# Kernel optimization log

Hardware: AMD Instinct MI355X
Metric: run time of the kernel (lower is better)

Reference implementation:

```python
import jax, jax.numpy as jnp
import numpy as np

EMBED_DIM = 128
TEMP_DIM = EMBED_DIM // 4  # 32
NUM_TYPES = 50
DATE_SCALE = 1825.0
LN_EPS = 1e-5


def _layernorm(x, w, b):
    m = jnp.mean(x, axis=-1, keepdims=True)
    v = jnp.mean((x - m) ** 2, axis=-1, keepdims=True)
    return (x - m) * jax.lax.rsqrt(v + LN_EPS) * w + b


def setup_inputs() -> dict:
    key = jax.random.key(0)
    ks = jax.random.split(key, 16)
    B, L = 4096, 200
    inp = {
        "treatment_ids": jax.random.randint(ks[0], (B, L), 0, NUM_TYPES, dtype=jnp.int64 if jax.config.jax_enable_x64 else jnp.int32),
        "dates": jax.random.uniform(ks[1], (B, L), dtype=jnp.float32) * DATE_SCALE,
        "lengths": jax.random.randint(ks[2], (B,), 0, L + 1, dtype=jnp.int32),
        # parameters
        "emb": jax.random.normal(ks[3], (NUM_TYPES, EMBED_DIM), jnp.float32),
        "tp_w": jax.random.normal(ks[4], (1, TEMP_DIM), jnp.float32) * 0.1,
        "tp_b": jnp.zeros((TEMP_DIM,), jnp.float32),
        "tp_lnw": jnp.ones((TEMP_DIM,), jnp.float32),
        "tp_lnb": jnp.zeros((TEMP_DIM,), jnp.float32),
        "w1": jax.random.normal(ks[5], (EMBED_DIM + TEMP_DIM, EMBED_DIM), jnp.float32) * 0.05,
        "b1": jnp.zeros((EMBED_DIM,), jnp.float32),
        "ln1w": jnp.ones((EMBED_DIM,), jnp.float32),
        "ln1b": jnp.zeros((EMBED_DIM,), jnp.float32),
        "w2": jax.random.normal(ks[6], (EMBED_DIM, EMBED_DIM), jnp.float32) * 0.05,
        "b2": jnp.zeros((EMBED_DIM,), jnp.float32),
        "ln2w": jnp.ones((EMBED_DIM,), jnp.float32),
        "ln2b": jnp.zeros((EMBED_DIM,), jnp.float32),
    }
    return inp


def reference(treatment_ids, dates, lengths, emb, tp_w, tp_b, tp_lnw, tp_lnb,
              w1, b1, ln1w, ln1b, w2, b2, ln2w, ln2b):
    B, L = treatment_ids.shape
    mask = (jnp.arange(L)[None, :] < lengths[:, None]).astype(dates.dtype)  # [B, L]

    # embedding lookup [B, L, D]
    treat = emb[treatment_ids]

    # temporal projection: Linear(1 -> D/4) + LN + GELU
    dn = (dates / DATE_SCALE)[..., None]                      # [B, L, 1]
    temporal = dn * tp_w[0] + tp_b                            # [B, L, D/4]
    temporal = jax.nn.gelu(_layernorm(temporal, tp_lnw, tp_lnb), approximate=False)

    combined = jnp.concatenate([treat, temporal], axis=-1)    # [B, L, D + D/4]

    # sequence encoder (dropout is identity at eval)
    h = jnp.einsum("blk,kd->bld", combined, w1) + b1
    h = jax.nn.gelu(_layernorm(h, ln1w, ln1b), approximate=False)
    h = jnp.einsum("blk,kd->bld", h, w2) + b2
    h = _layernorm(h, ln2w, ln2b)                             # [B, L, D]

    # masked mean pool; empty histories -> zeros
    counts = jnp.sum(mask, axis=1, keepdims=True)             # [B, 1]
    pooled = jnp.sum(h * mask[..., None], axis=1) / jnp.maximum(counts, 1.0)
    return jnp.where(counts > 0, pooled, 0.0)                 # [B, D]
```

## Files before the change

kernel.cpp:

```cpp
#include <hip/hip_runtime.h>
#include <cmath>

#define LN_EPS 1e-5f

typedef float  f32x4  __attribute__((ext_vector_type(4)));
typedef short  short8 __attribute__((ext_vector_type(8)));
typedef unsigned int uint4v __attribute__((ext_vector_type(4)));

#define W1TF_U4 512
#define W2F_U4  2048
#define E1_U4   1650
#define WLDS_U4 2560

__device__ __forceinline__ unsigned short f32_bf16_rne(float f) {
    union { float f; unsigned u; } v; v.f = f;
    unsigned r = v.u + 0x7FFFu + ((v.u >> 16) & 1u);
    return (unsigned short)(r >> 16);
}

__device__ __forceinline__ unsigned cvt_pk_bf16(float lo, float hi) {
    unsigned r;
    asm("v_cvt_pk_bf16_f32 %0, %1, %2" : "=v"(r) : "v"(lo), "v"(hi));
    return r;
}

__device__ __forceinline__ float gelu_f(float x) {
    float ax = fabsf(x);
    float a  = ax * 0.70710678118654752f;
    float t  = __builtin_amdgcn_rcpf(fmaf(0.3275911f, a, 1.0f));
    float p  = t * fmaf(t, fmaf(t, fmaf(t, fmaf(t, 1.061405429f, -1.453152027f),
                                        1.421413741f), -0.284496736f), 0.254829592f);
    float e  = __builtin_amdgcn_exp2f(-1.44269504089f * a * a);
    float E  = fmaf(-p, e, 1.0f);
    return 0.5f * fmaf(ax, E, x);
}

template<int C>
__device__ __forceinline__ float dpp_radd(float x) {
    int t = __builtin_amdgcn_update_dpp(0, __builtin_bit_cast(int, x), C, 0xF, 0xF, true);
    return x + __builtin_bit_cast(float, t);
}
__device__ __forceinline__ float red16(float x) {
    x = dpp_radd<0x128>(x);
    x = dpp_radd<0x124>(x);
    x = dpp_radd<0x122>(x);
    x = dpp_radd<0x121>(x);
    return x;
}

__global__ void prep_kernel(const float* __restrict__ w1, const float* __restrict__ w2,
                            const float* __restrict__ emb,
                            const float* __restrict__ tp_w, const float* __restrict__ tp_b,
                            unsigned* __restrict__ ws) {
    const int tid = blockIdx.x * 256 + threadIdx.x;
    uint4v* w1tf = (uint4v*)ws;
    uint4v* w2f  = w1tf + W1TF_U4;
    float*  E1   = (float*)(w2f + W2F_U4);
    float*  tps  = E1 + 6600;

    for (int i = tid; i < W1TF_U4; i += 8192) {
        const int lane = i & 63, nt = i >> 6;
        const int k0 = 128 + (lane >> 4) * 8, n = nt * 16 + (lane & 15);
        uint4v r;
        #pragma unroll
        for (int j2 = 0; j2 < 4; ++j2) {
            unsigned lo = f32_bf16_rne(w1[(k0 + 2 * j2) * 128 + n]);
            unsigned hi = f32_bf16_rne(w1[(k0 + 2 * j2 + 1) * 128 + n]);
            r[j2] = lo | (hi << 16);
        }
        w1tf[i] = r;
    }
    for (int i = tid; i < W2F_U4; i += 8192) {
        const int lane = i & 63, nt = (i >> 6) & 7, kt = i >> 9;
        const int k0 = kt * 32 + (lane >> 4) * 8, n = nt * 16 + (lane & 15);
        uint4v r;
        #pragma unroll
        for (int j2 = 0; j2 < 4; ++j2) {
            unsigned lo = f32_bf16_rne(w2[(k0 + 2 * j2) * 128 + n]);
            unsigned hi = f32_bf16_rne(w2[(k0 + 2 * j2 + 1) * 128 + n]);
            r[j2] = lo | (hi << 16);
        }
        w2f[i] = r;
    }
    if (tid < 6400) {
        const int t = tid >> 7, n = tid & 127;
        float s = 0.f;
        #pragma unroll 4
        for (int k = 0; k < 128; ++k)
            s = fmaf(emb[t * 128 + k], w1[k * 128 + n], s);
        E1[t * 132 + n] = s;
    }
    if (tid == 0) {
        float Sw = 0.f, Sb = 0.f, Sww = 0.f, Swb = 0.f, Sbb = 0.f;
        for (int j = 0; j < 32; ++j) {
            const float ww = tp_w[j], bb = tp_b[j];
            Sw += ww; Sb += bb; Sww += ww * ww; Swb += ww * bb; Sbb += bb * bb;
        }
        tps[0] = Sw; tps[1] = Sb; tps[2] = Sww; tps[3] = Swb; tps[4] = Sbb;
    }
}

__global__ __launch_bounds__(1024, 4) void encoder_mfma(
    const int*   __restrict__ tids,  const float* __restrict__ dates,
    const int*   __restrict__ lengths,
    const float* __restrict__ tp_w,  const float* __restrict__ tp_b,
    const float* __restrict__ tp_lnw,const float* __restrict__ tp_lnb,
    const float* __restrict__ b1,    const float* __restrict__ ln1w, const float* __restrict__ ln1b,
    const float* __restrict__ b2,    const float* __restrict__ ln2w, const float* __restrict__ ln2b,
    const unsigned* __restrict__ ws, float* __restrict__ out,
    int B, int L)
{
    __shared__ __align__(16) uint4v wlds[WLDS_U4];
    __shared__ __align__(16) float  E1lds[6600];
    __shared__ __align__(16) unsigned short a2[16][4][64][8];
    __shared__ float poolrow[4][128];
    __shared__ __align__(16) f32x4 tcoef[32];
    __shared__ __align__(16) f32x4 ecoef1[128];
    __shared__ __align__(16) f32x4 ecoef2[128];

    const int tid = threadIdx.x;
    const int lane = tid & 63, w = tid >> 6;
    const int c = lane & 15, g = lane >> 4;
    const int b0 = blockIdx.x * 4;

    for (int i = tid; i < WLDS_U4; i += 1024)
        wlds[i] = ((const uint4v*)ws)[i];
    for (int i = tid; i < E1_U4; i += 1024)
        ((uint4v*)E1lds)[i] = ((const uint4v*)ws)[WLDS_U4 + i];
    if (tid < 512) poolrow[tid >> 7][tid & 127] = 0.f;

    const float* tps = (const float*)((const uint4v*)ws + WLDS_U4 + E1_U4);

    if (tid < 32)  tcoef[tid]  = (f32x4){tp_w[tid], tp_b[tid], tp_lnw[tid], tp_lnb[tid]};
    if (tid < 128) {
        ecoef1[tid] = (f32x4){b1[tid], ln1w[tid], ln1b[tid], 0.f};
        ecoef2[tid] = (f32x4){b2[tid], ln2w[tid], ln2b[tid], 0.f};
    }
    __syncthreads();

    const float Sw = tps[0], Sb = tps[1], Sww = tps[2], Swb = tps[3], Sbb = tps[4];

    const int len0 = (b0 + 0 < B) ? min(max(lengths[b0 + 0], 0), L) : 0;
    const int len1 = (b0 + 1 < B) ? min(max(lengths[b0 + 1], 0), L) : 0;
    const int len2 = (b0 + 2 < B) ? min(max(lengths[b0 + 2], 0), L) : 0;
    const int len3 = (b0 + 3 < B) ? min(max(lengths[b0 + 3], 0), L) : 0;
    const int nt0 = (len0 + 15) >> 4, nt1 = (len1 + 15) >> 4;
    const int nt2 = (len2 + 15) >> 4, nt3 = (len3 + 15) >> 4;
    const int cum1 = nt0, cum2 = nt0 + nt1, cum3 = cum2 + nt2, T = cum3 + nt3;

    const int srl = lane ^ ((lane >> 3) & 3);

    for (int t = w; t < T; t += 16) {
        int row, tl, lenr;
        if (t >= cum3)      { row = 3; tl = t - cum3; lenr = len3; }
        else if (t >= cum2) { row = 2; tl = t - cum2; lenr = len2; }
        else if (t >= cum1) { row = 1; tl = t - cum1; lenr = len1; }
        else                { row = 0; tl = t;        lenr = len0; }
        const int R0 = tl << 4;
        const long base = (long)(b0 + row) * L;

        const int pc = min(R0 + c, L - 1);
        const float d = dates[base + pc] * (1.f / 1825.f);
        int idr[4];
        #pragma unroll
        for (int r = 0; r < 4; ++r)
            idr[r] = tids[base + min(R0 + 4 * g + r, L - 1)];

        short8 tfrag;
        {
            const float tm = fmaf(d, Sw, Sb) * (1.f / 32.f);
            float tv = fmaf(d * d, Sww, fmaf(2.f * d, Swb, Sbb)) * (1.f / 32.f) - tm * tm;
            const float trs = rsqrtf(fmaxf(tv, 0.f) + LN_EPS);
            const int j0 = g * 8;
            uint4v r;
            #pragma unroll
            for (int j2 = 0; j2 < 4; ++j2) {
                const f32x4 t0 = tcoef[j0 + 2*j2];
                const f32x4 t1 = tcoef[j0 + 2*j2 + 1];
                const float y0 = fmaf((fmaf(d, t0[0], t0[1]) - tm) * trs, t0[2], t0[3]);
                const float y1 = fmaf((fmaf(d, t1[0], t1[1]) - tm) * trs, t1[2], t1[3]);
                r[j2] = cvt_pk_bf16(gelu_f(y0), gelu_f(y1));
            }
            union { uint4v u; short8 s; } cv; cv.u = r;
            tfrag = cv.s;
        }

        f32x4 acc[8];
        #pragma unroll
        for (int r = 0; r < 4; ++r) {
            const int e1base = idr[r] * 132 + c;
            #pragma unroll
            for (int nt = 0; nt < 8; ++nt)
                acc[nt][r] = E1lds[e1base + nt * 16];
        }
        __builtin_amdgcn_s_setprio(1);
        #pragma unroll
        for (int nt = 0; nt < 8; ++nt) {
            const short8 bf = ((const short8*)wlds)[nt * 64 + lane];
            acc[nt] = __builtin_amdgcn_mfma_f32_16x16x32_bf16(tfrag, bf, acc[nt], 0, 0, 0);
        }
        __builtin_amdgcn_s_setprio(0);

        {
            f32x4 e1[8];
            #pragma unroll
            for (int nt = 0; nt < 8; ++nt) e1[nt] = ecoef1[nt * 16 + c];
            #pragma unroll
            for (int r = 0; r < 4; ++r) {
                float v[8], s = 0.f, q = 0.f;
                #pragma unroll
                for (int nt = 0; nt < 8; ++nt) {
                    v[nt] = acc[nt][r] + e1[nt][0];
                    s += v[nt]; q = fmaf(v[nt], v[nt], q);
                }
                s = red16(s); q = red16(q);
                const float mean = s * (1.f / 128.f);
                const float var  = fmaxf(q * (1.f / 128.f) - mean * mean, 0.f);
                const float rstd = rsqrtf(var + LN_EPS);
                const int mrow = 4 * g + r;
                #pragma unroll
                for (int n2 = 0; n2 < 4; ++n2) {
                    const float y0 = gelu_f(fmaf((v[2*n2]   - mean) * rstd, e1[2*n2][1],   e1[2*n2][2]));
                    const float y1 = gelu_f(fmaf((v[2*n2+1] - mean) * rstd, e1[2*n2+1][1], e1[2*n2+1][2]));
                    const unsigned pk = cvt_pk_bf16(y0, y1);
                    {
                        const int kcol  = (2*n2) * 16 + c;
                        const int row64 = ((kcol >> 3) & 3) * 16 + mrow;
                        const int srow  = row64 ^ ((row64 >> 3) & 3);
                        a2[w][kcol >> 5][srow][kcol & 7] = (unsigned short)(pk & 0xffffu);
                    }
                    {
                        const int kcol  = (2*n2+1) * 16 + c;
                        const int row64 = ((kcol >> 3) & 3) * 16 + mrow;
                        const int srow  = row64 ^ ((row64 >> 3) & 3);
                        a2[w][kcol >> 5][srow][kcol & 7] = (unsigned short)(pk >> 16);
                    }
                }
            }
        }

        asm volatile("" ::: "memory");

        f32x4 acc2[8];
        #pragma unroll
        for (int nt = 0; nt < 8; ++nt) acc2[nt] = (f32x4){0.f, 0.f, 0.f, 0.f};
        __builtin_amdgcn_s_setprio(1);
        #pragma unroll
        for (int kt2 = 0; kt2 < 4; ++kt2) {
            short8 af;
            __builtin_memcpy(&af, &a2[w][kt2][srl][0], 16);
            #pragma unroll
            for (int nt = 0; nt < 8; ++nt) {
                const short8 bf = ((const short8*)(wlds + W1TF_U4))[(kt2 * 8 + nt) * 64 + lane];
                acc2[nt] = __builtin_amdgcn_mfma_f32_16x16x32_bf16(af, bf, acc2[nt], 0, 0, 0);
            }
        }
        __builtin_amdgcn_s_setprio(0);

        asm volatile("" ::: "memory");

        {
            f32x4 e2[8];
            #pragma unroll
            for (int nt = 0; nt < 8; ++nt) e2[nt] = ecoef2[nt * 16 + c];
            float ptile[8];
            #pragma unroll
            for (int nt = 0; nt < 8; ++nt) ptile[nt] = 0.f;
            #pragma unroll
            for (int r = 0; r < 4; ++r) {
                float v[8], s = 0.f, q = 0.f;
                #pragma unroll
                for (int nt = 0; nt < 8; ++nt) {
                    v[nt] = acc2[nt][r] + e2[nt][0];
                    s += v[nt]; q = fmaf(v[nt], v[nt], q);
                }
                s = red16(s); q = red16(q);
                const float mean = s * (1.f / 128.f);
                const float var  = fmaxf(q * (1.f / 128.f) - mean * mean, 0.f);
                const float rstd = rsqrtf(var + LN_EPS);
                const float msk = ((R0 + 4 * g + r) < lenr) ? 1.f : 0.f;
                #pragma unroll
                for (int nt = 0; nt < 8; ++nt) {
                    const float y = fmaf((v[nt] - mean) * rstd, e2[nt][1], e2[nt][2]);
                    ptile[nt] = fmaf(y, msk, ptile[nt]);
                }
            }
            #pragma unroll
            for (int nt = 0; nt < 8; ++nt) {
                float tv = ptile[nt];
                tv += __shfl_xor(tv, 16);
                tv += __shfl_xor(tv, 32);
                ptile[nt] = tv;
            }
            if (g == 0) {
                #pragma unroll
                for (int nt = 0; nt < 8; ++nt)
                    atomicAdd(&poolrow[row][nt * 16 + c], ptile[nt]);
            }
        }
    }

    __syncthreads();
    if (tid < 512) {
        const int r4  = tid >> 7;
        const int col = tid & 127;
        const int bo  = b0 + r4;
        if (bo < B) {
            const int lenb = min(max(lengths[bo], 0), L);
            out[bo * 128 + col] = (lenb > 0) ? poolrow[r4][col] / (float)lenb : 0.f;
        }
    }
}

extern "C" void kernel_launch(void* const* d_in, const int* in_sizes, int n_in,
                              void* d_out, int out_size, void* d_ws, size_t ws_size,
                              hipStream_t stream) {
    const int*   tids    = (const int*)  d_in[0];
    const float* dates   = (const float*)d_in[1];
    const int*   lengths = (const int*)  d_in[2];
    const float* emb     = (const float*)d_in[3];
    const float* tp_w    = (const float*)d_in[4];
    const float* tp_b    = (const float*)d_in[5];
    const float* tp_lnw  = (const float*)d_in[6];
    const float* tp_lnb  = (const float*)d_in[7];
    const float* w1      = (const float*)d_in[8];
    const float* b1      = (const float*)d_in[9];
    const float* ln1w    = (const float*)d_in[10];
    const float* ln1b    = (const float*)d_in[11];
    const float* w2      = (const float*)d_in[12];
    const float* b2      = (const float*)d_in[13];
    const float* ln2w    = (const float*)d_in[14];
    const float* ln2b    = (const float*)d_in[15];
    float* out = (float*)d_out;

    const int B = in_sizes[2];
    const int L = in_sizes[0] / B;

    hipLaunchKernelGGL(prep_kernel, dim3(32), dim3(256), 0, stream,
                       w1, w2, emb, tp_w, tp_b, (unsigned*)d_ws);
    hipLaunchKernelGGL(encoder_mfma, dim3((B + 3) / 4), dim3(1024), 0, stream,
                       tids, dates, lengths, tp_w, tp_b, tp_lnw, tp_lnb,
                       b1, ln1w, ln1b, b2, ln2w, ln2b,
                       (const unsigned*)d_ws, out, B, L);
}
```

Measured before the change: 217.0 us.

## Process 32-row tiles per wave, read E1 from global, use 768-thread blocks

Each wave now handles two 16-row M-tiles per iteration, so every B-fragment load from LDS feeds two MFMAs. The E1 table (embedding times W1) moves out of LDS and is gathered from global/L2 with stride 128. Blocks shrink to 768 threads covering 6 batch rows, with the a2 staging buffer doubled per wave. This is meant to cut LDS pressure and raise weight reuse, at the cost of more registers per wave, padding waste on the 32-row tiles, and uncached global gathers for E1.

```diff
diff --git a/kernel.cpp b/kernel.cpp
--- a/kernel.cpp
+++ b/kernel.cpp
@@ -9,7 +9,7 @@
 
 #define W1TF_U4 512
 #define W2F_U4  2048
-#define E1_U4   1650
+#define E1_U4   1600
 #define WLDS_U4 2560
 
 __device__ __forceinline__ unsigned short f32_bf16_rne(float f) {
@@ -56,7 +56,7 @@
     uint4v* w1tf = (uint4v*)ws;
     uint4v* w2f  = w1tf + W1TF_U4;
     float*  E1   = (float*)(w2f + W2F_U4);
-    float*  tps  = E1 + 6600;
+    float*  tps  = E1 + 6400;
 
     for (int i = tid; i < W1TF_U4; i += 8192) {
         const int lane = i & 63, nt = i >> 6;
@@ -88,7 +88,7 @@
         #pragma unroll 4
         for (int k = 0; k < 128; ++k)
             s = fmaf(emb[t * 128 + k], w1[k * 128 + n], s);
-        E1[t * 132 + n] = s;
+        E1[t * 128 + n] = s;
     }
     if (tid == 0) {
         float Sw = 0.f, Sb = 0.f, Sww = 0.f, Swb = 0.f, Sbb = 0.f;
@@ -100,7 +100,7 @@
     }
 }
 
-__global__ __launch_bounds__(1024, 4) void encoder_mfma(
+__global__ __launch_bounds__(768, 3) void encoder_mfma(
     const int*   __restrict__ tids,  const float* __restrict__ dates,
     const int*   __restrict__ lengths,
     const float* __restrict__ tp_w,  const float* __restrict__ tp_b,
@@ -111,9 +111,8 @@
     int B, int L)
 {
     __shared__ __align__(16) uint4v wlds[WLDS_U4];
-    __shared__ __align__(16) float  E1lds[6600];
-    __shared__ __align__(16) unsigned short a2[16][4][64][8];
-    __shared__ float poolrow[4][128];
+    __shared__ __align__(16) unsigned short a2[12][2][4][64][8];
+    __shared__ float poolrow[6][128];
     __shared__ __align__(16) f32x4 tcoef[32];
     __shared__ __align__(16) f32x4 ecoef1[128];
     __shared__ __align__(16) f32x4 ecoef2[128];
@@ -121,15 +120,14 @@
     const int tid = threadIdx.x;
     const int lane = tid & 63, w = tid >> 6;
     const int c = lane & 15, g = lane >> 4;
-    const int b0 = blockIdx.x * 4;
-
-    for (int i = tid; i < WLDS_U4; i += 1024)
+    const int b0 = blockIdx.x * 6;
+
+    for (int i = tid; i < WLDS_U4; i += 768)
         wlds[i] = ((const uint4v*)ws)[i];
-    for (int i = tid; i < E1_U4; i += 1024)
-        ((uint4v*)E1lds)[i] = ((const uint4v*)ws)[WLDS_U4 + i];
-    if (tid < 512) poolrow[tid >> 7][tid & 127] = 0.f;
-
-    const float* tps = (const float*)((const uint4v*)ws + WLDS_U4 + E1_U4);
+    poolrow[tid >> 7][tid & 127] = 0.f;
+
+    const float* E1g = (const float*)((const uint4v*)ws + WLDS_U4);
+    const float* tps = E1g + 6400;
 
     if (tid < 32)  tcoef[tid]  = (f32x4){tp_w[tid], tp_b[tid], tp_lnw[tid], tp_lnb[tid]};
     if (tid < 128) {
@@ -140,64 +138,93 @@
 
     const float Sw = tps[0], Sb = tps[1], Sww = tps[2], Swb = tps[3], Sbb = tps[4];
 
-    const int len0 = (b0 + 0 < B) ? min(max(lengths[b0 + 0], 0), L) : 0;
-    const int len1 = (b0 + 1 < B) ? min(max(lengths[b0 + 1], 0), L) : 0;
-    const int len2 = (b0 + 2 < B) ? min(max(lengths[b0 + 2], 0), L) : 0;
-    const int len3 = (b0 + 3 < B) ? min(max(lengths[b0 + 3], 0), L) : 0;
-    const int nt0 = (len0 + 15) >> 4, nt1 = (len1 + 15) >> 4;
-    const int nt2 = (len2 + 15) >> 4, nt3 = (len3 + 15) >> 4;
-    const int cum1 = nt0, cum2 = nt0 + nt1, cum3 = cum2 + nt2, T = cum3 + nt3;
+    int lenA[6];
+    #pragma unroll
+    for (int i = 0; i < 6; ++i)
+        lenA[i] = (b0 + i < B) ? min(max(lengths[b0 + i], 0), L) : 0;
+    const int n0 = (lenA[0] + 31) >> 5, n1 = (lenA[1] + 31) >> 5, n2 = (lenA[2] + 31) >> 5;
+    const int n3 = (lenA[3] + 31) >> 5, n4 = (lenA[4] + 31) >> 5, n5 = (lenA[5] + 31) >> 5;
+    const int cum1 = n0, cum2 = cum1 + n1, cum3 = cum2 + n2;
+    const int cum4 = cum3 + n3, cum5 = cum4 + n4, T = cum5 + n5;
+    const int len0 = lenA[0], len1 = lenA[1], len2 = lenA[2];
+    const int len3 = lenA[3], len4 = lenA[4], len5 = lenA[5];
 
     const int srl = lane ^ ((lane >> 3) & 3);
 
-    for (int t = w; t < T; t += 16) {
+    for (int st = w; st < T; st += 12) {
         int row, tl, lenr;
-        if (t >= cum3)      { row = 3; tl = t - cum3; lenr = len3; }
-        else if (t >= cum2) { row = 2; tl = t - cum2; lenr = len2; }
-        else if (t >= cum1) { row = 1; tl = t - cum1; lenr = len1; }
-        else                { row = 0; tl = t;        lenr = len0; }
-        const int R0 = tl << 4;
+        if      (st >= cum5) { row = 5; tl = st - cum5; lenr = len5; }
+        else if (st >= cum4) { row = 4; tl = st - cum4; lenr = len4; }
+        else if (st >= cum3) { row = 3; tl = st - cum3; lenr = len3; }
+        else if (st >= cum2) { row = 2; tl = st - cum2; lenr = len2; }
+        else if (st >= cum1) { row = 1; tl = st - cum1; lenr = len1; }
+        else                 { row = 0; tl = st;        lenr = len0; }
+        const int R0 = tl << 5;
+        const bool amt1 = (R0 + 16) < lenr;
         const long base = (long)(b0 + row) * L;
 
-        const int pc = min(R0 + c, L - 1);
-        const float d = dates[base + pc] * (1.f / 1825.f);
-        int idr[4];
+        int idr0[4], idr1[4];
         #pragma unroll
         for (int r = 0; r < 4; ++r)
-            idr[r] = tids[base + min(R0 + 4 * g + r, L - 1)];
-
-        short8 tfrag;
+            idr0[r] = tids[base + min(R0 + 4 * g + r, L - 1)];
+        if (amt1) {
+            #pragma unroll
+            for (int r = 0; r < 4; ++r)
+                idr1[r] = tids[base + min(R0 + 16 + 4 * g + r, L - 1)];
+        }
+        const float dn0 = dates[base + min(R0 + c,      L - 1)] * (1.f / 1825.f);
+        const float dn1 = dates[base + min(R0 + 16 + c, L - 1)] * (1.f / 1825.f);
+
+        f32x4 acc[2][8];
+        #pragma unroll
+        for (int r = 0; r < 4; ++r) {
+            const int e1b = idr0[r] * 128 + c;
+            #pragma unroll
+            for (int nt = 0; nt < 8; ++nt)
+                acc[0][nt][r] = E1g[e1b + nt * 16];
+        }
+        if (amt1) {
+            #pragma unroll
+            for (int r = 0; r < 4; ++r) {
+                const int e1b = idr1[r] * 128 + c;
+                #pragma unroll
+                for (int nt = 0; nt < 8; ++nt)
+                    acc[1][nt][r] = E1g[e1b + nt * 16];
+            }
+        }
+
+        short8 tfrag[2];
         {
-            const float tm = fmaf(d, Sw, Sb) * (1.f / 32.f);
-            float tv = fmaf(d * d, Sww, fmaf(2.f * d, Swb, Sbb)) * (1.f / 32.f) - tm * tm;
-            const float trs = rsqrtf(fmaxf(tv, 0.f) + LN_EPS);
             const int j0 = g * 8;
-            uint4v r;
-            #pragma unroll
-            for (int j2 = 0; j2 < 4; ++j2) {
-                const f32x4 t0 = tcoef[j0 + 2*j2];
-                const f32x4 t1 = tcoef[j0 + 2*j2 + 1];
-                const float y0 = fmaf((fmaf(d, t0[0], t0[1]) - tm) * trs, t0[2], t0[3]);
-                const float y1 = fmaf((fmaf(d, t1[0], t1[1]) - tm) * trs, t1[2], t1[3]);
-                r[j2] = cvt_pk_bf16(gelu_f(y0), gelu_f(y1));
-            }
-            union { uint4v u; short8 s; } cv; cv.u = r;
-            tfrag = cv.s;
-        }
-
-        f32x4 acc[8];
-        #pragma unroll
-        for (int r = 0; r < 4; ++r) {
-            const int e1base = idr[r] * 132 + c;
-            #pragma unroll
-            for (int nt = 0; nt < 8; ++nt)
-                acc[nt][r] = E1lds[e1base + nt * 16];
-        }
+            f32x4 tc[8];
+            #pragma unroll
+            for (int jj = 0; jj < 8; ++jj) tc[jj] = tcoef[j0 + jj];
+            #pragma unroll
+            for (int mt = 0; mt < 2; ++mt) {
+                const float d  = mt ? dn1 : dn0;
+                const float tm = fmaf(d, Sw, Sb) * (1.f / 32.f);
+                float tv = fmaf(d * d, Sww, fmaf(2.f * d, Swb, Sbb)) * (1.f / 32.f) - tm * tm;
+                const float trs = rsqrtf(fmaxf(tv, 0.f) + LN_EPS);
+                uint4v r;
+                #pragma unroll
+                for (int j2 = 0; j2 < 4; ++j2) {
+                    const f32x4 t0 = tc[2*j2], t1 = tc[2*j2 + 1];
+                    const float y0 = fmaf((fmaf(d, t0[0], t0[1]) - tm) * trs, t0[2], t0[3]);
+                    const float y1 = fmaf((fmaf(d, t1[0], t1[1]) - tm) * trs, t1[2], t1[3]);
+                    r[j2] = cvt_pk_bf16(gelu_f(y0), gelu_f(y1));
+                }
+                union { uint4v u; short8 s; } cv; cv.u = r;
+                tfrag[mt] = cv.s;
+            }
+        }
+
         __builtin_amdgcn_s_setprio(1);
         #pragma unroll
         for (int nt = 0; nt < 8; ++nt) {
             const short8 bf = ((const short8*)wlds)[nt * 64 + lane];
-            acc[nt] = __builtin_amdgcn_mfma_f32_16x16x32_bf16(tfrag, bf, acc[nt], 0, 0, 0);
+            acc[0][nt] = __builtin_amdgcn_mfma_f32_16x16x32_bf16(tfrag[0], bf, acc[0][nt], 0, 0, 0);
+            if (amt1)
+                acc[1][nt] = __builtin_amdgcn_mfma_f32_16x16x32_bf16(tfrag[1], bf, acc[1][nt], 0, 0, 0);
         }
         __builtin_amdgcn_s_setprio(0);
 
@@ -206,34 +233,38 @@
             #pragma unroll
             for (int nt = 0; nt < 8; ++nt) e1[nt] = ecoef1[nt * 16 + c];
             #pragma unroll
-            for (int r = 0; r < 4; ++r) {
-                float v[8], s = 0.f, q = 0.f;
-                #pragma unroll
-                for (int nt = 0; nt < 8; ++nt) {
-                    v[nt] = acc[nt][r] + e1[nt][0];
-                    s += v[nt]; q = fmaf(v[nt], v[nt], q);
-                }
-                s = red16(s); q = red16(q);
-                const float mean = s * (1.f / 128.f);
-                const float var  = fmaxf(q * (1.f / 128.f) - mean * mean, 0.f);
-                const float rstd = rsqrtf(var + LN_EPS);
-                const int mrow = 4 * g + r;
-                #pragma unroll
-                for (int n2 = 0; n2 < 4; ++n2) {
-                    const float y0 = gelu_f(fmaf((v[2*n2]   - mean) * rstd, e1[2*n2][1],   e1[2*n2][2]));
-                    const float y1 = gelu_f(fmaf((v[2*n2+1] - mean) * rstd, e1[2*n2+1][1], e1[2*n2+1][2]));
-                    const unsigned pk = cvt_pk_bf16(y0, y1);
-                    {
-                        const int kcol  = (2*n2) * 16 + c;
-                        const int row64 = ((kcol >> 3) & 3) * 16 + mrow;
-                        const int srow  = row64 ^ ((row64 >> 3) & 3);
-                        a2[w][kcol >> 5][srow][kcol & 7] = (unsigned short)(pk & 0xffffu);
+            for (int mt = 0; mt < 2; ++mt) {
+                if (mt && !amt1) continue;
+                #pragma unroll
+                for (int r = 0; r < 4; ++r) {
+                    float v[8], s = 0.f, q = 0.f;
+                    #pragma unroll
+                    for (int nt = 0; nt < 8; ++nt) {
+                        v[nt] = acc[mt][nt][r] + e1[nt][0];
+                        s += v[nt]; q = fmaf(v[nt], v[nt], q);
                     }
-                    {
-                        const int kcol  = (2*n2+1) * 16 + c;
-                        const int row64 = ((kcol >> 3) & 3) * 16 + mrow;
-                        const int srow  = row64 ^ ((row64 >> 3) & 3);
-                        a2[w][kcol >> 5][srow][kcol & 7] = (unsigned short)(pk >> 16);
+                    s = red16(s); q = red16(q);
+                    const float mean = s * (1.f / 128.f);
+                    const float var  = fmaxf(q * (1.f / 128.f) - mean * mean, 0.f);
+                    const float rstd = rsqrtf(var + LN_EPS);
+                    const int mrow = 4 * g + r;
+                    #pragma unroll
+                    for (int n2 = 0; n2 < 4; ++n2) {
+                        const float y0 = gelu_f(fmaf((v[2*n2]   - mean) * rstd, e1[2*n2][1],   e1[2*n2][2]));
+                        const float y1 = gelu_f(fmaf((v[2*n2+1] - mean) * rstd, e1[2*n2+1][1], e1[2*n2+1][2]));
+                        const unsigned pk = cvt_pk_bf16(y0, y1);
+                        {
+                            const int kcol  = (2*n2) * 16 + c;
+                            const int row64 = ((kcol >> 3) & 3) * 16 + mrow;
+                            const int srow  = row64 ^ ((row64 >> 3) & 3);
+                            a2[w][mt][kcol >> 5][srow][kcol & 7] = (unsigned short)(pk & 0xffffu);
+                        }
+                        {
+                            const int kcol  = (2*n2+1) * 16 + c;
+                            const int row64 = ((kcol >> 3) & 3) * 16 + mrow;
+                            const int srow  = row64 ^ ((row64 >> 3) & 3);
+                            a2[w][mt][kcol >> 5][srow][kcol & 7] = (unsigned short)(pk >> 16);
+                        }
                     }
                 }
             }
@@ -241,18 +272,23 @@
 
         asm volatile("" ::: "memory");
 
-        f32x4 acc2[8];
-        #pragma unroll
-        for (int nt = 0; nt < 8; ++nt) acc2[nt] = (f32x4){0.f, 0.f, 0.f, 0.f};
+        f32x4 acc2[2][8];
+        #pragma unroll
+        for (int mt = 0; mt < 2; ++mt)
+            #pragma unroll
+            for (int nt = 0; nt < 8; ++nt) acc2[mt][nt] = (f32x4){0.f, 0.f, 0.f, 0.f};
         __builtin_amdgcn_s_setprio(1);
         #pragma unroll
         for (int kt2 = 0; kt2 < 4; ++kt2) {
-            short8 af;
-            __builtin_memcpy(&af, &a2[w][kt2][srl][0], 16);
+            short8 af0, af1;
+            __builtin_memcpy(&af0, &a2[w][0][kt2][srl][0], 16);
+            if (amt1) __builtin_memcpy(&af1, &a2[w][1][kt2][srl][0], 16);
             #pragma unroll
             for (int nt = 0; nt < 8; ++nt) {
                 const short8 bf = ((const short8*)(wlds + W1TF_U4))[(kt2 * 8 + nt) * 64 + lane];
-                acc2[nt] = __builtin_amdgcn_mfma_f32_16x16x32_bf16(af, bf, acc2[nt], 0, 0, 0);
+                acc2[0][nt] = __builtin_amdgcn_mfma_f32_16x16x32_bf16(af0, bf, acc2[0][nt], 0, 0, 0);
+                if (amt1)
+                    acc2[1][nt] = __builtin_amdgcn_mfma_f32_16x16x32_bf16(af1, bf, acc2[1][nt], 0, 0, 0);
             }
         }
         __builtin_amdgcn_s_setprio(0);
@@ -267,22 +303,26 @@
             #pragma unroll
             for (int nt = 0; nt < 8; ++nt) ptile[nt] = 0.f;
             #pragma unroll
-            for (int r = 0; r < 4; ++r) {
-                float v[8], s = 0.f, q = 0.f;
-                #pragma unroll
-                for (int nt = 0; nt < 8; ++nt) {
-                    v[nt] = acc2[nt][r] + e2[nt][0];
-                    s += v[nt]; q = fmaf(v[nt], v[nt], q);
-                }
-                s = red16(s); q = red16(q);
-                const float mean = s * (1.f / 128.f);
-                const float var  = fmaxf(q * (1.f / 128.f) - mean * mean, 0.f);
-                const float rstd = rsqrtf(var + LN_EPS);
-                const float msk = ((R0 + 4 * g + r) < lenr) ? 1.f : 0.f;
-                #pragma unroll
-                for (int nt = 0; nt < 8; ++nt) {
-                    const float y = fmaf((v[nt] - mean) * rstd, e2[nt][1], e2[nt][2]);
-                    ptile[nt] = fmaf(y, msk, ptile[nt]);
+            for (int mt = 0; mt < 2; ++mt) {
+                if (mt && !amt1) continue;
+                #pragma unroll
+                for (int r = 0; r < 4; ++r) {
+                    float v[8], s = 0.f, q = 0.f;
+                    #pragma unroll
+                    for (int nt = 0; nt < 8; ++nt) {
+                        v[nt] = acc2[mt][nt][r] + e2[nt][0];
+                        s += v[nt]; q = fmaf(v[nt], v[nt], q);
+                    }
+                    s = red16(s); q = red16(q);
+                    const float mean = s * (1.f / 128.f);
+                    const float var  = fmaxf(q * (1.f / 128.f) - mean * mean, 0.f);
+                    const float rstd = rsqrtf(var + LN_EPS);
+                    const float msk = ((R0 + mt * 16 + 4 * g + r) < lenr) ? 1.f : 0.f;
+                    #pragma unroll
+                    for (int nt = 0; nt < 8; ++nt) {
+                        const float y = fmaf((v[nt] - mean) * rstd, e2[nt][1], e2[nt][2]);
+                        ptile[nt] = fmaf(y, msk, ptile[nt]);
+                    }
                 }
             }
             #pragma unroll
@@ -301,13 +341,13 @@
     }
 
     __syncthreads();
-    if (tid < 512) {
-        const int r4  = tid >> 7;
+    {
+        const int r6  = tid >> 7;
         const int col = tid & 127;
-        const int bo  = b0 + r4;
+        const int bo  = b0 + r6;
         if (bo < B) {
             const int lenb = min(max(lengths[bo], 0), L);
-            out[bo * 128 + col] = (lenb > 0) ? poolrow[r4][col] / (float)lenb : 0.f;
+            out[bo * 128 + col] = (lenb > 0) ? poolrow[r6][col] / (float)lenb : 0.f;
         }
     }
 }
@@ -338,7 +378,7 @@
 
     hipLaunchKernelGGL(prep_kernel, dim3(32), dim3(256), 0, stream,
                        w1, w2, emb, tp_w, tp_b, (unsigned*)d_ws);
-    hipLaunchKernelGGL(encoder_mfma, dim3((B + 3) / 4), dim3(1024), 0, stream,
+    hipLaunchKernelGGL(encoder_mfma, dim3((B + 5) / 6), dim3(768), 0, stream,
                        tids, dates, lengths, tp_w, tp_b, tp_lnw, tp_lnb,
                        b1, ln1w, ln1b, b2, ln2w, ln2b,
                        (const unsigned*)d_ws, out, B, L);
```

New measurement: 227.2 us. +4.7%, slower.
